# Kernel tuning notes

Hardware: AMD Instinct MI355X
Metric: run time of the kernel (lower is better)

## Reference

```python
import jax, jax.numpy as jnp
import numpy as np

TOTAL_ATOMS = 204800
NUM_GRAPHS = 4096
NUM_FEATURES = 128
MAX_ATOMS = 128  # static upper bound on per-graph atom count


def setup_inputs() -> dict:
    key = jax.random.key(0)
    kx, kb = jax.random.split(key)
    x = jax.random.normal(kx, (TOTAL_ATOMS, NUM_FEATURES), dtype=jnp.float32)
    batch_ids = jnp.sort(jax.random.randint(kb, (TOTAL_ATOMS,), 0, NUM_GRAPHS)).astype(jnp.int64)
    return {"x": x, "batch_ids": batch_ids, "num_graphs": NUM_GRAPHS, "max_num_atoms": MAX_ATOMS}


def reference(x, batch_ids, num_graphs, max_num_atoms):
    # x: [N, F] ragged atom features; batch_ids: [N] sorted graph ids.
    N = x.shape[0]
    counts = jnp.bincount(batch_ids, length=num_graphs)            # [G]
    starts = jnp.cumsum(counts) - counts                            # [G] start offset of each graph
    pos = jnp.arange(N) - starts[batch_ids]                         # within-graph atom position
    result = jnp.zeros((num_graphs, max_num_atoms, x.shape[1]), dtype=x.dtype)
    result = result.at[batch_ids, pos].set(x, mode="drop")         # single fused scatter
    mask = jnp.arange(max_num_atoms)[None, :] < counts[:, None]     # [G, M] bool
    return result, mask
```

## Files before the change

kernel.cpp:

```cpp
#include <hip/hip_runtime.h>
#include <hip/hip_bf16.h>


constexpr int kF  = 128;
constexpr int kM  = 128;
constexpr int kG  = 4096;
constexpr int kF4 = kF / 4;

constexpr int kThreads    = 256;
constexpr int kFillBlocks = 4096;
constexpr int kResF4      = kG * kM * kF4;
constexpr int kMaskF4     = kG * kM / 4;
constexpr int kIters      = kResF4 / (kThreads * kFillBlocks);

typedef float fx4 __attribute__((ext_vector_type(4)));

__global__ void starts_kernel(const int* __restrict__ bids, int N,
                              int* __restrict__ starts) {
    int i = blockIdx.x * blockDim.x + threadIdx.x;
    if (i >= N) return;
    int b    = bids[i];
    int prev = (i == 0) ? -1 : bids[i - 1];
    for (int g = prev + 1; g <= b; ++g) starts[g] = i;
    if (i == N - 1) {
        for (int g = b + 1; g <= kG; ++g) starts[g] = N;
    }
}

__global__ __launch_bounds__(kThreads)
void fill_kernel(const fx4* __restrict__ x4,
                 const int* __restrict__ starts,
                 fx4* __restrict__ out4,
                 fx4* __restrict__ mask4) {
    const int base = blockIdx.x * kThreads + threadIdx.x;
#pragma unroll
    for (int it = 0; it < kIters; ++it) {
        const int i    = base + it * (kThreads * kFillBlocks);
        const int lane = i & (kF4 - 1);
        const int row  = i >> 5;
        const int p    = row & (kM - 1);
        const int g    = row >> 7;
        const int s0   = starts[g];
        const int s1   = starts[g + 1];
        fx4 v = (fx4)(0.f);
        if (p < s1 - s0) {
            v = __builtin_nontemporal_load(&x4[(s0 + p) * kF4 + lane]);
        }
        __builtin_nontemporal_store(v, &out4[i]);
    }
    if (base < kMaskF4) {
        const int g  = base >> 5;
        const int p0 = (base & 31) << 2;
        const int c  = starts[g + 1] - starts[g];
        fx4 v;
        v.x = (p0 + 0 < c) ? 1.f : 0.f;
        v.y = (p0 + 1 < c) ? 1.f : 0.f;
        v.z = (p0 + 2 < c) ? 1.f : 0.f;
        v.w = (p0 + 3 < c) ? 1.f : 0.f;
        __builtin_nontemporal_store(v, &mask4[base]);
    }
}

extern "C" void kernel_launch(void* const* d_in, const int* in_sizes, int n_in,
                              void* d_out, int out_size, void* d_ws, size_t ws_size,
                              hipStream_t stream) {
    const float* x    = (const float*)d_in[0];
    const int*   bids = (const int*)d_in[1];
    const int    N    = in_sizes[0] / kF;

    float* out = (float*)d_out;
    int* starts = (int*)d_ws;

    starts_kernel<<<(N + kThreads - 1) / kThreads, kThreads, 0, stream>>>(bids, N, starts);

    fx4* mask4 = (fx4*)(out + (long long)kG * kM * kF);
    fill_kernel<<<kFillBlocks, kThreads, 0, stream>>>((const fx4*)x, starts,
                                                      (fx4*)out, mask4);
}
```

Measured before the change: 357.6 us.

## Fuse graph start computation into fill kernel via wave-parallel binary search

Removes the separate starts kernel and launch. Each block now handles one graph, and two wavefronts find the graph's start and end offsets with a 64-way ballot-based search over the sorted batch ids. The fill loop then writes one contiguous slab per block using a count held in a register, with no per-element reads of the starts array. Every block pays a few dependent global-memory search rounds before it begins streaming, which could delay the memory-bound copy.

```diff
diff --git a/kernel.cpp b/kernel.cpp
--- a/kernel.cpp
+++ b/kernel.cpp
@@ -6,58 +6,68 @@
 constexpr int kM  = 128;
 constexpr int kG  = 4096;
 constexpr int kF4 = kF / 4;
-
-constexpr int kThreads    = 256;
-constexpr int kFillBlocks = 4096;
-constexpr int kResF4      = kG * kM * kF4;
-constexpr int kMaskF4     = kG * kM / 4;
-constexpr int kIters      = kResF4 / (kThreads * kFillBlocks);
+constexpr int kSlabF4 = kM * kF4;
 
 typedef float fx4 __attribute__((ext_vector_type(4)));
 
-__global__ void starts_kernel(const int* __restrict__ bids, int N,
-                              int* __restrict__ starts) {
-    int i = blockIdx.x * blockDim.x + threadIdx.x;
-    if (i >= N) return;
-    int b    = bids[i];
-    int prev = (i == 0) ? -1 : bids[i - 1];
-    for (int g = prev + 1; g <= b; ++g) starts[g] = i;
-    if (i == N - 1) {
-        for (int g = b + 1; g <= kG; ++g) starts[g] = N;
+__device__ __forceinline__ int wave_lower_bound(const int* __restrict__ bids,
+                                                int N, int T, int lane) {
+    int lo = -1, hi = N;
+    while (hi - lo > 1) {
+        const long long count = hi - lo - 1;
+        const int pos = lo + 1 + (int)(((long long)lane * count) >> 6);
+        const bool pred = (bids[pos] >= T);
+        const unsigned long long bal = __ballot(pred);
+        if (bal == 0) {
+            lo = lo + 1 + (int)((63LL * count) >> 6);
+        } else {
+            const int j = __ffsll(bal) - 1;
+            hi = lo + 1 + (int)(((long long)j * count) >> 6);
+            if (j > 0)
+                lo = lo + 1 + (int)(((long long)(j - 1) * count) >> 6);
+        }
     }
+    return hi;
 }
 
-__global__ __launch_bounds__(kThreads)
-void fill_kernel(const fx4* __restrict__ x4,
-                 const int* __restrict__ starts,
-                 fx4* __restrict__ out4,
-                 fx4* __restrict__ mask4) {
-    const int base = blockIdx.x * kThreads + threadIdx.x;
+__global__ __launch_bounds__(256)
+void fused_kernel(const fx4* __restrict__ x4, const int* __restrict__ bids,
+                  int N, fx4* __restrict__ out4, fx4* __restrict__ mask4) {
+    const int g   = blockIdx.x;
+    const int tid = threadIdx.x;
+    __shared__ int sh[2];
+
+    if (tid < 128) {
+        const int which = tid >> 6;
+        const int lane  = tid & 63;
+        const int r = wave_lower_bound(bids, N, g + which, lane);
+        if (lane == 0) sh[which] = r;
+    }
+    __syncthreads();
+    const int s0 = sh[0];
+    const int c  = sh[1] - s0;
+
+    fx4* slab = out4 + ((long long)g << 12);
 #pragma unroll
-    for (int it = 0; it < kIters; ++it) {
-        const int i    = base + it * (kThreads * kFillBlocks);
-        const int lane = i & (kF4 - 1);
-        const int row  = i >> 5;
-        const int p    = row & (kM - 1);
-        const int g    = row >> 7;
-        const int s0   = starts[g];
-        const int s1   = starts[g + 1];
+    for (int it = 0; it < kSlabF4 / 256; ++it) {
+        const int idx  = it * 256 + tid;
+        const int row  = idx >> 5;
+        const int lane = idx & (kF4 - 1);
         fx4 v = (fx4)(0.f);
-        if (p < s1 - s0) {
-            v = __builtin_nontemporal_load(&x4[(s0 + p) * kF4 + lane]);
+        if (row < c) {
+            v = __builtin_nontemporal_load(&x4[(s0 + row) * kF4 + lane]);
         }
-        __builtin_nontemporal_store(v, &out4[i]);
+        __builtin_nontemporal_store(v, &slab[idx]);
     }
-    if (base < kMaskF4) {
-        const int g  = base >> 5;
-        const int p0 = (base & 31) << 2;
-        const int c  = starts[g + 1] - starts[g];
+
+    if (tid < 32) {
+        const int p0 = tid << 2;
         fx4 v;
         v.x = (p0 + 0 < c) ? 1.f : 0.f;
         v.y = (p0 + 1 < c) ? 1.f : 0.f;
         v.z = (p0 + 2 < c) ? 1.f : 0.f;
         v.w = (p0 + 3 < c) ? 1.f : 0.f;
-        __builtin_nontemporal_store(v, &mask4[base]);
+        __builtin_nontemporal_store(v, &mask4[(g << 5) + tid]);
     }
 }
 
@@ -68,12 +78,9 @@
     const int*   bids = (const int*)d_in[1];
     const int    N    = in_sizes[0] / kF;
 
-    float* out = (float*)d_out;
-    int* starts = (int*)d_ws;
+    float* out  = (float*)d_out;
+    fx4* mask4  = (fx4*)(out + (long long)kG * kM * kF);
 
-    starts_kernel<<<(N + kThreads - 1) / kThreads, kThreads, 0, stream>>>(bids, N, starts);
-
-    fx4* mask4 = (fx4*)(out + (long long)kG * kM * kF);
-    fill_kernel<<<kFillBlocks, kThreads, 0, stream>>>((const fx4*)x, starts,
-                                                      (fx4*)out, mask4);
+    fused_kernel<<<kG, 256, 0, stream>>>((const fx4*)x, bids, N,
+                                         (fx4*)out, mask4);
 }
```

After: 342.5 us. 4.2% less time.
